# Optimization experiments

Measured on AMD Instinct MI355X. Metric: run time of the kernel, lower is better.

## Reference

```python
import jax, jax.numpy as jnp
import numpy as np

D_MODEL = 1024
N_HEADS = 16
D_K = D_MODEL // N_HEADS


def setup_inputs() -> dict:
    key = jax.random.key(0)
    ks = jax.random.split(key, 11)
    B, S = 2, 2048
    scale = 1.0 / np.sqrt(D_MODEL)
    return {
        "query": jax.random.normal(ks[0], (B, S, D_MODEL), jnp.float32),
        "key": jax.random.normal(ks[1], (B, S, D_MODEL), jnp.float32),
        "value": jax.random.normal(ks[2], (B, S, D_MODEL), jnp.float32),
        "w_q": jax.random.normal(ks[3], (D_MODEL, D_MODEL), jnp.float32) * scale,
        "b_q": jnp.zeros((D_MODEL,), jnp.float32),
        "w_k": jax.random.normal(ks[4], (D_MODEL, D_MODEL), jnp.float32) * scale,
        "b_k": jnp.zeros((D_MODEL,), jnp.float32),
        "w_v": jax.random.normal(ks[5], (D_MODEL, D_MODEL), jnp.float32) * scale,
        "b_v": jnp.zeros((D_MODEL,), jnp.float32),
        "w_o": jax.random.normal(ks[6], (D_MODEL, D_MODEL), jnp.float32) * scale,
        "b_o": jnp.zeros((D_MODEL,), jnp.float32),
    }


def reference(query, key, value, w_q, b_q, w_k, b_k, w_v, b_v, w_o, b_o):
    B, S, _ = query.shape
    # Linear projections (torch Linear: x @ W.T + b), split heads -> (B, H, S, Dk)
    def proj(x, w, b):
        y = jnp.einsum('bsd,ed->bse', x, w) + b
        return y.reshape(B, -1, N_HEADS, D_K).transpose(0, 2, 1, 3)
    q = proj(query, w_q, b_q)
    k = proj(key, w_k, b_k)
    v = proj(value, w_v, b_v)
    # Scaled dot-product attention (full O(S^2) scores, faithful to source)
    scores = jnp.einsum('bhqd,bhkd->bhqk', q, k) / np.sqrt(D_K)
    attn = jax.nn.softmax(scores, axis=-1)
    out = jnp.einsum('bhqk,bhkd->bhqd', attn, v)  # (B, H, S, Dk)
    out = out.transpose(0, 2, 1, 3).reshape(B, S, D_MODEL)
    out = jnp.einsum('bsd,ed->bse', out, w_o) + b_o
    return out
```

## Files before the change

### kernel.cpp

```cpp
#include <hip/hip_runtime.h>
#include <hip/hip_bf16.h>

#define DM 1024
#define NH 16
#define DKH 64
#define BB 2
#define SS 2048
#define MM (BB*SS)
#define HKB 1024

typedef __bf16 v8bf __attribute__((ext_vector_type(8)));
typedef float  v4f  __attribute__((ext_vector_type(4)));
typedef float  v16f __attribute__((ext_vector_type(16)));

__device__ __forceinline__ unsigned short f2bf(float f) {
    union { float f; unsigned int u; } v; v.f = f;
    unsigned int u = v.u;
    unsigned int r = (u + 0x7fffu + ((u >> 16) & 1u)) >> 16;
    return (unsigned short)r;
}

__device__ __forceinline__ int cvtpk(float lo, float hi) {
    int r;
    asm("v_cvt_pk_bf16_f32 %0, %1, %2" : "=v"(r) : "v"(lo), "v"(hi));
    return r;
}

__device__ __forceinline__ void pl32swap(int& a, int& b) {
    asm("v_permlane32_swap_b32 %0, %1" : "+v"(a), "+v"(b));
}

__device__ __forceinline__ void gl16(const unsigned short* g, unsigned short* l) {
    auto gp = reinterpret_cast<const __attribute__((address_space(1))) unsigned int*>(
        reinterpret_cast<uintptr_t>(g));
    auto lp = reinterpret_cast<__attribute__((address_space(3))) unsigned int*>(
        reinterpret_cast<uintptr_t>(l));
    __builtin_amdgcn_global_load_lds(gp, lp, 16, 0, 0);
}

__global__ __launch_bounds__(256) void cvt_to_bf16(
    const float* __restrict__ xq, const float* __restrict__ xk, const float* __restrict__ xv,
    const float* __restrict__ wq, const float* __restrict__ wk, const float* __restrict__ wv,
    const float* __restrict__ wo, unsigned short* __restrict__ dst)
{
    const int y = blockIdx.y;
    const float* src;
    size_t n, off;
    if (y < 3) {
        src = (y == 0) ? xq : (y == 1) ? xk : xv;
        n = (size_t)MM * DM;
        off = (size_t)y * MM * DM;
    } else {
        src = (y == 3) ? wq : (y == 4) ? wk : (y == 5) ? wv : wo;
        n = (size_t)DM * DM;
        off = (size_t)3 * MM * DM + (size_t)(y - 3) * DM * DM;
    }
    unsigned short* d = dst + off;
    const size_t stride = (size_t)gridDim.x * blockDim.x;
    for (size_t i = (size_t)blockIdx.x * blockDim.x + threadIdx.x; i * 8 < n; i += stride) {
        float4 a = ((const float4*)src)[2 * i];
        float4 b = ((const float4*)src)[2 * i + 1];
        uint4 o;
        o.x = (unsigned)cvtpk(a.x, a.y);
        o.y = (unsigned)cvtpk(a.z, a.w);
        o.z = (unsigned)cvtpk(b.x, b.y);
        o.w = (unsigned)cvtpk(b.z, b.w);
        ((uint4*)d)[i] = o;
    }
}

__global__ __launch_bounds__(256) void proj_qkv_b(
    const unsigned short* __restrict__ xb, const unsigned short* __restrict__ wb,
    const float* __restrict__ bq, const float* __restrict__ bk, const float* __restrict__ bv,
    unsigned short* __restrict__ q_ws, unsigned short* __restrict__ k_ws,
    unsigned short* __restrict__ vt_ws)
{
    const int z = blockIdx.z;
    const unsigned short* X = xb + (size_t)z * MM * DM;
    const unsigned short* W = wb + (size_t)z * DM * DM;
    const float* bias = (z == 0) ? bq : (z == 1) ? bk : bv;

    __shared__ unsigned short lA[2][128 * 32];
    __shared__ unsigned short lB[2][128 * 32];

    const int t = threadIdx.x;
    const int lane = t & 63, w = t >> 6;
    const int wm = w >> 1, wn = w & 1;
    const int g = lane >> 4, lr = lane & 15;

    const int hid = blockIdx.y * 8 + blockIdx.x;
    const int xcd = hid & 7, slot = hid >> 3;
    const int mbase = (xcd * 4 + (slot & 3)) * 128;
    const int nbase = (slot >> 2) * 128;

    const int srow = lane >> 2;
    const int scol = (lane & 3) * 8;

    v4f acc[4][4];
#pragma unroll
    for (int i = 0; i < 4; ++i)
#pragma unroll
        for (int j = 0; j < 4; ++j)
            acc[i][j] = (v4f){0.f, 0.f, 0.f, 0.f};

    auto stage = [&](int bi, int kb) {
        gl16(X + (size_t)(mbase + w * 16 + srow) * DM + kb + scol,      &lA[bi][w * 512]);
        gl16(X + (size_t)(mbase + 64 + w * 16 + srow) * DM + kb + scol, &lA[bi][(w + 4) * 512]);
        gl16(W + (size_t)(nbase + w * 16 + srow) * DM + kb + scol,      &lB[bi][w * 512]);
        gl16(W + (size_t)(nbase + 64 + w * 16 + srow) * DM + kb + scol, &lB[bi][(w + 4) * 512]);
    };

    stage(0, 0);
    __syncthreads();
    int buf = 0;
    for (int ki = 0; ki < 32; ++ki) {
        if (ki + 1 < 32) stage(buf ^ 1, (ki + 1) * 32);

        v8bf af[4], bf4[4];
#pragma unroll
        for (int mt = 0; mt < 4; ++mt)
            af[mt] = *(const v8bf*)(&lA[buf][(wm * 64 + mt * 16 + lr) * 32 + g * 8]);
#pragma unroll
        for (int nt = 0; nt < 4; ++nt)
            bf4[nt] = *(const v8bf*)(&lB[buf][(wn * 64 + nt * 16 + lr) * 32 + g * 8]);
#pragma unroll
        for (int mt = 0; mt < 4; ++mt)
#pragma unroll
            for (int nt = 0; nt < 4; ++nt)
                acc[mt][nt] = __builtin_amdgcn_mfma_f32_16x16x32_bf16(af[mt], bf4[nt], acc[mt][nt], 0, 0, 0);

        __syncthreads();
        buf ^= 1;
    }

    const float scale = (z == 0) ? 0.18033688011112042f : 1.0f;
#pragma unroll
    for (int nt = 0; nt < 4; ++nt) {
        int e = nbase + wn * 64 + nt * 16 + lr;
        float bval = bias[e];
        int h = e >> 6, dk = e & 63;
#pragma unroll
        for (int mt = 0; mt < 4; ++mt) {
#pragma unroll
            for (int r = 0; r < 4; ++r) {
                int m = mbase + wm * 64 + mt * 16 + g * 4 + r;
                float val = (acc[mt][nt][r] + bval) * scale;
                unsigned short o = f2bf(val);
                int b = m >> 11, s = m & 2047;
                if (z == 2) {
                    vt_ws[((size_t)(b * NH + h) * DKH + dk) * SS + s] = o;
                } else {
                    unsigned short* dst = (z == 0) ? q_ws : k_ws;
                    dst[((size_t)(b * NH + h) * SS + s) * DKH + dk] = o;
                }
            }
        }
    }
}

#define KB 64
#define LDP 72
#define TILE 4608

__global__ __launch_bounds__(512, 4) void attn_kernel(
    const unsigned short* __restrict__ q_ws, const unsigned short* __restrict__ k_ws,
    const unsigned short* __restrict__ vt_ws, unsigned short* __restrict__ o_ws)
{
    __shared__ __align__(16) unsigned short lsBuf[2 * 4 * TILE];

    const int t = threadIdx.x, l = t & 63, w = t >> 6;
    const int h = l >> 5, ql = l & 31;
    const int qg = w >> 1, hf = w & 1;

    const int hid = blockIdx.x;
    const int slot = hid >> 3;
    const int bh = (hid & 7) * 4 + (slot & 3);
    const int qp = slot >> 2;
    const int q0 = qp * 128 + qg * 32;

    const unsigned short* Kb = k_ws + (size_t)bh * SS * DKH;
    const unsigned short* Vb = vt_ws + (size_t)bh * DKH * SS;

    v8bf qf[4];
#pragma unroll
    for (int c = 0; c < 4; ++c)
        qf[c] = *(const v8bf*)(q_ws + ((size_t)bh * SS + q0 + ql) * DKH + c * 16 + h * 8);

    v16f oT[2];
#pragma unroll
    for (int d = 0; d < 2; ++d)
#pragma unroll
        for (int r = 0; r < 16; ++r) oT[d][r] = 0.f;
    float l_lane = 0.f;
    const v16f z16 = {};

    const int r0s = t >> 3, c0s = (t & 7) * 8;
    uint4 k0r, k1r, v0r, v1r;

    k0r = *(const uint4*)(Kb + (size_t)(r0s) * DKH + c0s);
    v0r = *(const uint4*)(Vb + (size_t)r0s * SS + c0s);
    k1r = *(const uint4*)(Kb + (size_t)(HKB + r0s) * DKH + c0s);
    v1r = *(const uint4*)(Vb + (size_t)r0s * SS + HKB + c0s);
    {
        unsigned short* B0 = lsBuf;
        *(uint4*)&B0[0 * TILE + r0s * LDP + c0s] = k0r;
        *(uint4*)&B0[1 * TILE + r0s * LDP + c0s] = v0r;
        *(uint4*)&B0[2 * TILE + r0s * LDP + c0s] = k1r;
        *(uint4*)&B0[3 * TILE + r0s * LDP + c0s] = v1r;
    }
    k0r = *(const uint4*)(Kb + (size_t)(KB + r0s) * DKH + c0s);
    v0r = *(const uint4*)(Vb + (size_t)r0s * SS + KB + c0s);
    k1r = *(const uint4*)(Kb + (size_t)(HKB + KB + r0s) * DKH + c0s);
    v1r = *(const uint4*)(Vb + (size_t)r0s * SS + HKB + KB + c0s);
    __syncthreads();

    const int NT = 16;
    int p = 0;
    for (int tt = 0; tt < NT; ++tt) {
        unsigned short* Kp = lsBuf + p * (4 * TILE) + hf * (2 * TILE);
        unsigned short* Vp = Kp + TILE;
        if (tt + 1 < NT) {
            unsigned short* Bn = lsBuf + (p ^ 1) * (4 * TILE);
            *(uint4*)&Bn[0 * TILE + r0s * LDP + c0s] = k0r;
            *(uint4*)&Bn[1 * TILE + r0s * LDP + c0s] = v0r;
            *(uint4*)&Bn[2 * TILE + r0s * LDP + c0s] = k1r;
            *(uint4*)&Bn[3 * TILE + r0s * LDP + c0s] = v1r;
        }
        if (tt + 2 < NT) {
            int kt2 = (tt + 2) * KB;
            k0r = *(const uint4*)(Kb + (size_t)(kt2 + r0s) * DKH + c0s);
            v0r = *(const uint4*)(Vb + (size_t)r0s * SS + kt2 + c0s);
            k1r = *(const uint4*)(Kb + (size_t)(HKB + kt2 + r0s) * DKH + c0s);
            v1r = *(const uint4*)(Vb + (size_t)r0s * SS + HKB + kt2 + c0s);
        }

        v16f sT[2];
        __builtin_amdgcn_s_setprio(1);
#pragma unroll
        for (int kb = 0; kb < 2; ++kb) {
            v8bf kf = *(const v8bf*)&Kp[(kb * 32 + ql) * LDP + h * 8];
            sT[kb] = __builtin_amdgcn_mfma_f32_32x32x16_bf16(kf, qf[0], z16, 0, 0, 0);
        }
#pragma unroll
        for (int c = 1; c < 4; ++c)
#pragma unroll
            for (int kb = 0; kb < 2; ++kb) {
                v8bf kf = *(const v8bf*)&Kp[(kb * 32 + ql) * LDP + c * 16 + h * 8];
                sT[kb] = __builtin_amdgcn_mfma_f32_32x32x16_bf16(kf, qf[c], sT[kb], 0, 0, 0);
            }
        __builtin_amdgcn_s_setprio(0);

        float rs0 = 0.f, rs1 = 0.f, rs2 = 0.f, rs3 = 0.f;
#pragma unroll
        for (int kb = 0; kb < 2; ++kb)
#pragma unroll
            for (int r = 0; r < 16; r += 4) {
                float e0 = __builtin_amdgcn_exp2f(sT[kb][r + 0]);
                float e1 = __builtin_amdgcn_exp2f(sT[kb][r + 1]);
                float e2 = __builtin_amdgcn_exp2f(sT[kb][r + 2]);
                float e3 = __builtin_amdgcn_exp2f(sT[kb][r + 3]);
                sT[kb][r + 0] = e0; sT[kb][r + 1] = e1;
                sT[kb][r + 2] = e2; sT[kb][r + 3] = e3;
                rs0 += e0; rs1 += e1; rs2 += e2; rs3 += e3;
            }
        l_lane += (rs0 + rs1) + (rs2 + rs3);

        v8bf pfrag[4];
#pragma unroll
        for (int c = 0; c < 4; ++c) {
            const int cc = c & 1, kb = c >> 1;
            int A0 = cvtpk(sT[kb][8 * cc + 0], sT[kb][8 * cc + 1]);
            int A1 = cvtpk(sT[kb][8 * cc + 2], sT[kb][8 * cc + 3]);
            int B0 = cvtpk(sT[kb][8 * cc + 4], sT[kb][8 * cc + 5]);
            int B1 = cvtpk(sT[kb][8 * cc + 6], sT[kb][8 * cc + 7]);
            pl32swap(A0, B0);
            pl32swap(A1, B1);
            union { int i[4]; v8bf v; } u;
            u.i[0] = A0; u.i[1] = A1; u.i[2] = B0; u.i[3] = B1;
            pfrag[c] = u.v;
        }

        __builtin_amdgcn_s_setprio(1);
#pragma unroll
        for (int db = 0; db < 2; ++db)
#pragma unroll
            for (int c = 0; c < 4; ++c) {
                v8bf vf = *(const v8bf*)&Vp[(db * 32 + ql) * LDP + c * 16 + h * 8];
                oT[db] = __builtin_amdgcn_mfma_f32_32x32x16_bf16(vf, pfrag[c], oT[db], 0, 0, 0);
            }
        __builtin_amdgcn_s_setprio(0);

        __syncthreads();
        p ^= 1;
    }

    float lsum = l_lane + __shfl_xor(l_lane, 32);
    float* lsf = (float*)lsBuf;
    const int row = qg * 32 + ql;
#pragma unroll
    for (int db = 0; db < 2; ++db)
#pragma unroll
        for (int r = 0; r < 16; ++r) {
            int d = db * 32 + (r & 3) + 8 * (r >> 2) + 4 * h;
            lsf[(hf * 128 + row) * 65 + d] = oT[db][r];
        }
    if (h == 0) lsf[(hf * 128 + row) * 65 + 64] = lsum;
    __syncthreads();

    const int orow = t >> 2;
    const int ck = t & 3;
    const float* e0 = lsf + orow * 65;
    const float* e1 = lsf + (128 + orow) * 65;
    const float linv = 1.0f / (e0[64] + e1[64]);
    const int b = bh >> 4, hh = bh & 15;
    const int d0 = ck * 16;
    unsigned short* op = o_ws + ((size_t)b * SS + qp * 128 + orow) * DM + hh * DKH + d0;
    uint4 o0, o1;
    o0.x = (unsigned)cvtpk((e0[d0+0]+e1[d0+0])*linv,  (e0[d0+1]+e1[d0+1])*linv);
    o0.y = (unsigned)cvtpk((e0[d0+2]+e1[d0+2])*linv,  (e0[d0+3]+e1[d0+3])*linv);
    o0.z = (unsigned)cvtpk((e0[d0+4]+e1[d0+4])*linv,  (e0[d0+5]+e1[d0+5])*linv);
    o0.w = (unsigned)cvtpk((e0[d0+6]+e1[d0+6])*linv,  (e0[d0+7]+e1[d0+7])*linv);
    o1.x = (unsigned)cvtpk((e0[d0+8]+e1[d0+8])*linv,  (e0[d0+9]+e1[d0+9])*linv);
    o1.y = (unsigned)cvtpk((e0[d0+10]+e1[d0+10])*linv,(e0[d0+11]+e1[d0+11])*linv);
    o1.z = (unsigned)cvtpk((e0[d0+12]+e1[d0+12])*linv,(e0[d0+13]+e1[d0+13])*linv);
    o1.w = (unsigned)cvtpk((e0[d0+14]+e1[d0+14])*linv,(e0[d0+15]+e1[d0+15])*linv);
    *(uint4*)op = o0;
    *(uint4*)(op + 8) = o1;
}

__global__ __launch_bounds__(256) void proj_o_b(
    const unsigned short* __restrict__ A, const unsigned short* __restrict__ W,
    const float* __restrict__ bo, float* __restrict__ out)
{
    __shared__ unsigned short lA[2][128 * 32];
    __shared__ unsigned short lB[2][128 * 32];

    const int t = threadIdx.x;
    const int lane = t & 63, w = t >> 6;
    const int wm = w >> 1, wn = w & 1;
    const int g = lane >> 4, lr = lane & 15;

    const int hid = blockIdx.y * 8 + blockIdx.x;
    const int xcd = hid & 7, slot = hid >> 3;
    const int mbase = (xcd * 4 + (slot & 3)) * 128;
    const int nbase = (slot >> 2) * 128;

    const int srow = lane >> 2;
    const int scol = (lane & 3) * 8;

    v4f acc[4][4];
#pragma unroll
    for (int i = 0; i < 4; ++i)
#pragma unroll
        for (int j = 0; j < 4; ++j)
            acc[i][j] = (v4f){0.f, 0.f, 0.f, 0.f};

    auto stage = [&](int bi, int kb) {
        gl16(A + (size_t)(mbase + w * 16 + srow) * DM + kb + scol,      &lA[bi][w * 512]);
        gl16(A + (size_t)(mbase + 64 + w * 16 + srow) * DM + kb + scol, &lA[bi][(w + 4) * 512]);
        gl16(W + (size_t)(nbase + w * 16 + srow) * DM + kb + scol,      &lB[bi][w * 512]);
        gl16(W + (size_t)(nbase + 64 + w * 16 + srow) * DM + kb + scol, &lB[bi][(w + 4) * 512]);
    };

    stage(0, 0);
    __syncthreads();
    int buf = 0;
    for (int ki = 0; ki < 32; ++ki) {
        if (ki + 1 < 32) stage(buf ^ 1, (ki + 1) * 32);

        v8bf af[4], bf4[4];
#pragma unroll
        for (int mt = 0; mt < 4; ++mt)
            af[mt] = *(const v8bf*)(&lA[buf][(wm * 64 + mt * 16 + lr) * 32 + g * 8]);
#pragma unroll
        for (int nt = 0; nt < 4; ++nt)
            bf4[nt] = *(const v8bf*)(&lB[buf][(wn * 64 + nt * 16 + lr) * 32 + g * 8]);
#pragma unroll
        for (int mt = 0; mt < 4; ++mt)
#pragma unroll
            for (int nt = 0; nt < 4; ++nt)
                acc[mt][nt] = __builtin_amdgcn_mfma_f32_16x16x32_bf16(af[mt], bf4[nt], acc[mt][nt], 0, 0, 0);

        __syncthreads();
        buf ^= 1;
    }

#pragma unroll
    for (int nt = 0; nt < 4; ++nt) {
        int e = nbase + wn * 64 + nt * 16 + lr;
        float bval = bo[e];
#pragma unroll
        for (int mt = 0; mt < 4; ++mt) {
#pragma unroll
            for (int r = 0; r < 4; ++r) {
                int m = mbase + wm * 64 + mt * 16 + g * 4 + r;
                out[(size_t)m * DM + e] = acc[mt][nt][r] + bval;
            }
        }
    }
}

extern "C" void kernel_launch(void* const* d_in, const int* in_sizes, int n_in,
                              void* d_out, int out_size, void* d_ws, size_t ws_size,
                              hipStream_t stream) {
    const float* q  = (const float*)d_in[0];
    const float* k  = (const float*)d_in[1];
    const float* v  = (const float*)d_in[2];
    const float* wq = (const float*)d_in[3];
    const float* bq = (const float*)d_in[4];
    const float* wk = (const float*)d_in[5];
    const float* bk = (const float*)d_in[6];
    const float* wv = (const float*)d_in[7];
    const float* bv = (const float*)d_in[8];
    const float* wo = (const float*)d_in[9];
    const float* bo = (const float*)d_in[10];
    float* out = (float*)d_out;

    unsigned short* ws    = (unsigned short*)d_ws;
    unsigned short* q_ws  = ws;
    unsigned short* k_ws  = q_ws + (size_t)MM * DM;
    unsigned short* vt_ws = k_ws + (size_t)MM * DM;
    unsigned short* xb    = vt_ws + (size_t)MM * DM;
    unsigned short* wb    = xb + (size_t)3 * MM * DM;
    unsigned short* o_ws  = xb;

    cvt_to_bf16<<<dim3(256, 7), 256, 0, stream>>>(q, k, v, wq, wk, wv, wo, xb);
    proj_qkv_b<<<dim3(8, 32, 3), 256, 0, stream>>>(xb, wb, bq, bk, bv, q_ws, k_ws, vt_ws);
    attn_kernel<<<dim3(512), 512, 0, stream>>>(q_ws, k_ws, vt_ws, o_ws);
    proj_o_b<<<dim3(8, 32), 256, 0, stream>>>(o_ws, wb + (size_t)3 * DM * DM, bo, out);
}
```

Baseline: 128.8 us.

## Triple-buffer projection GEMM loads and halve output-projection N tile

Both projection GEMMs move from a double-buffered loop with a full __syncthreads per step to a three-stage LDS ring. Two tiles stay in flight, and explicit s_waitcnt vmcnt counts plus s_barrier wait only for the tile being consumed. The output projection also drops its N tile from 128 to 64 and launches twice as many blocks, so 256 blocks become 512 for better CU occupancy. The costs are more shared memory per block and lower per-block data reuse in the output projection. The correctness of the hand-counted vmcnt values depends on gl16 issuing exactly one vector memory op per call.

```diff
diff --git a/kernel.cpp b/kernel.cpp
--- a/kernel.cpp
+++ b/kernel.cpp
@@ -80,8 +80,8 @@
     const unsigned short* W = wb + (size_t)z * DM * DM;
     const float* bias = (z == 0) ? bq : (z == 1) ? bk : bv;
 
-    __shared__ unsigned short lA[2][128 * 32];
-    __shared__ unsigned short lB[2][128 * 32];
+    __shared__ unsigned short lA[3][128 * 32];
+    __shared__ unsigned short lB[3][128 * 32];
 
     const int t = threadIdx.x;
     const int lane = t & 63, w = t >> 6;
@@ -109,29 +109,50 @@
         gl16(W + (size_t)(nbase + w * 16 + srow) * DM + kb + scol,      &lB[bi][w * 512]);
         gl16(W + (size_t)(nbase + 64 + w * 16 + srow) * DM + kb + scol, &lB[bi][(w + 4) * 512]);
     };
-
-    stage(0, 0);
-    __syncthreads();
-    int buf = 0;
-    for (int ki = 0; ki < 32; ++ki) {
-        if (ki + 1 < 32) stage(buf ^ 1, (ki + 1) * 32);
-
+    auto compute = [&](int bi) {
         v8bf af[4], bf4[4];
 #pragma unroll
         for (int mt = 0; mt < 4; ++mt)
-            af[mt] = *(const v8bf*)(&lA[buf][(wm * 64 + mt * 16 + lr) * 32 + g * 8]);
+            af[mt] = *(const v8bf*)(&lA[bi][(wm * 64 + mt * 16 + lr) * 32 + g * 8]);
 #pragma unroll
         for (int nt = 0; nt < 4; ++nt)
-            bf4[nt] = *(const v8bf*)(&lB[buf][(wn * 64 + nt * 16 + lr) * 32 + g * 8]);
+            bf4[nt] = *(const v8bf*)(&lB[bi][(wn * 64 + nt * 16 + lr) * 32 + g * 8]);
 #pragma unroll
         for (int mt = 0; mt < 4; ++mt)
 #pragma unroll
             for (int nt = 0; nt < 4; ++nt)
                 acc[mt][nt] = __builtin_amdgcn_mfma_f32_16x16x32_bf16(af[mt], bf4[nt], acc[mt][nt], 0, 0, 0);
-
-        __syncthreads();
-        buf ^= 1;
-    }
+    };
+
+    stage(0, 0);
+    stage(1, 32);
+    int bcur = 0;
+#pragma unroll 1
+    for (int ki = 0; ki < 30; ++ki) {
+        int bnext = bcur + 2; if (bnext >= 3) bnext -= 3;
+        stage(bnext, (ki + 2) * 32);
+        asm volatile("s_waitcnt vmcnt(8)" ::: "memory");
+        __builtin_amdgcn_sched_barrier(0);
+        __builtin_amdgcn_s_barrier();
+        __builtin_amdgcn_sched_barrier(0);
+        compute(bcur);
+        __builtin_amdgcn_sched_barrier(0);
+        __builtin_amdgcn_s_barrier();
+        bcur = (bcur == 2) ? 0 : bcur + 1;
+    }
+    asm volatile("s_waitcnt vmcnt(4)" ::: "memory");
+    __builtin_amdgcn_sched_barrier(0);
+    __builtin_amdgcn_s_barrier();
+    __builtin_amdgcn_sched_barrier(0);
+    compute(bcur);
+    __builtin_amdgcn_sched_barrier(0);
+    __builtin_amdgcn_s_barrier();
+    bcur = (bcur == 2) ? 0 : bcur + 1;
+    asm volatile("s_waitcnt vmcnt(0)" ::: "memory");
+    __builtin_amdgcn_sched_barrier(0);
+    __builtin_amdgcn_s_barrier();
+    __builtin_amdgcn_sched_barrier(0);
+    compute(bcur);
 
     const float scale = (z == 0) ? 0.18033688011112042f : 1.0f;
 #pragma unroll
@@ -332,62 +353,82 @@
     const unsigned short* __restrict__ A, const unsigned short* __restrict__ W,
     const float* __restrict__ bo, float* __restrict__ out)
 {
-    __shared__ unsigned short lA[2][128 * 32];
-    __shared__ unsigned short lB[2][128 * 32];
+    __shared__ unsigned short lA[3][128 * 32];
+    __shared__ unsigned short lB[3][64 * 32];
 
     const int t = threadIdx.x;
     const int lane = t & 63, w = t >> 6;
     const int wm = w >> 1, wn = w & 1;
     const int g = lane >> 4, lr = lane & 15;
 
-    const int hid = blockIdx.y * 8 + blockIdx.x;
+    const int hid = blockIdx.y * 16 + blockIdx.x;
     const int xcd = hid & 7, slot = hid >> 3;
     const int mbase = (xcd * 4 + (slot & 3)) * 128;
-    const int nbase = (slot >> 2) * 128;
+    const int nbase = (slot >> 2) * 64;
 
     const int srow = lane >> 2;
     const int scol = (lane & 3) * 8;
 
-    v4f acc[4][4];
+    v4f acc[4][2];
 #pragma unroll
     for (int i = 0; i < 4; ++i)
 #pragma unroll
-        for (int j = 0; j < 4; ++j)
+        for (int j = 0; j < 2; ++j)
             acc[i][j] = (v4f){0.f, 0.f, 0.f, 0.f};
 
     auto stage = [&](int bi, int kb) {
         gl16(A + (size_t)(mbase + w * 16 + srow) * DM + kb + scol,      &lA[bi][w * 512]);
         gl16(A + (size_t)(mbase + 64 + w * 16 + srow) * DM + kb + scol, &lA[bi][(w + 4) * 512]);
         gl16(W + (size_t)(nbase + w * 16 + srow) * DM + kb + scol,      &lB[bi][w * 512]);
-        gl16(W + (size_t)(nbase + 64 + w * 16 + srow) * DM + kb + scol, &lB[bi][(w + 4) * 512]);
     };
+    auto compute = [&](int bi) {
+        v8bf af[4], bf4[2];
+#pragma unroll
+        for (int mt = 0; mt < 4; ++mt)
+            af[mt] = *(const v8bf*)(&lA[bi][(wm * 64 + mt * 16 + lr) * 32 + g * 8]);
+#pragma unroll
+        for (int nt = 0; nt < 2; ++nt)
+            bf4[nt] = *(const v8bf*)(&lB[bi][(wn * 32 + nt * 16 + lr) * 32 + g * 8]);
+#pragma unroll
+        for (int mt = 0; mt < 4; ++mt)
+#pragma unroll
+            for (int nt = 0; nt < 2; ++nt)
+                acc[mt][nt] = __builtin_amdgcn_mfma_f32_16x16x32_bf16(af[mt], bf4[nt], acc[mt][nt], 0, 0, 0);
+    };
 
     stage(0, 0);
-    __syncthreads();
-    int buf = 0;
-    for (int ki = 0; ki < 32; ++ki) {
-        if (ki + 1 < 32) stage(buf ^ 1, (ki + 1) * 32);
-
-        v8bf af[4], bf4[4];
-#pragma unroll
-        for (int mt = 0; mt < 4; ++mt)
-            af[mt] = *(const v8bf*)(&lA[buf][(wm * 64 + mt * 16 + lr) * 32 + g * 8]);
-#pragma unroll
-        for (int nt = 0; nt < 4; ++nt)
-            bf4[nt] = *(const v8bf*)(&lB[buf][(wn * 64 + nt * 16 + lr) * 32 + g * 8]);
-#pragma unroll
-        for (int mt = 0; mt < 4; ++mt)
-#pragma unroll
-            for (int nt = 0; nt < 4; ++nt)
-                acc[mt][nt] = __builtin_amdgcn_mfma_f32_16x16x32_bf16(af[mt], bf4[nt], acc[mt][nt], 0, 0, 0);
-
-        __syncthreads();
-        buf ^= 1;
-    }
-
-#pragma unroll
-    for (int nt = 0; nt < 4; ++nt) {
-        int e = nbase + wn * 64 + nt * 16 + lr;
+    stage(1, 32);
+    int bcur = 0;
+#pragma unroll 1
+    for (int ki = 0; ki < 30; ++ki) {
+        int bnext = bcur + 2; if (bnext >= 3) bnext -= 3;
+        stage(bnext, (ki + 2) * 32);
+        asm volatile("s_waitcnt vmcnt(6)" ::: "memory");
+        __builtin_amdgcn_sched_barrier(0);
+        __builtin_amdgcn_s_barrier();
+        __builtin_amdgcn_sched_barrier(0);
+        compute(bcur);
+        __builtin_amdgcn_sched_barrier(0);
+        __builtin_amdgcn_s_barrier();
+        bcur = (bcur == 2) ? 0 : bcur + 1;
+    }
+    asm volatile("s_waitcnt vmcnt(3)" ::: "memory");
+    __builtin_amdgcn_sched_barrier(0);
+    __builtin_amdgcn_s_barrier();
+    __builtin_amdgcn_sched_barrier(0);
+    compute(bcur);
+    __builtin_amdgcn_sched_barrier(0);
+    __builtin_amdgcn_s_barrier();
+    bcur = (bcur == 2) ? 0 : bcur + 1;
+    asm volatile("s_waitcnt vmcnt(0)" ::: "memory");
+    __builtin_amdgcn_sched_barrier(0);
+    __builtin_amdgcn_s_barrier();
+    __builtin_amdgcn_sched_barrier(0);
+    compute(bcur);
+
+#pragma unroll
+    for (int nt = 0; nt < 2; ++nt) {
+        int e = nbase + wn * 32 + nt * 16 + lr;
         float bval = bo[e];
 #pragma unroll
         for (int mt = 0; mt < 4; ++mt) {
@@ -427,5 +468,5 @@
     cvt_to_bf16<<<dim3(256, 7), 256, 0, stream>>>(q, k, v, wq, wk, wv, wo, xb);
     proj_qkv_b<<<dim3(8, 32, 3), 256, 0, stream>>>(xb, wb, bq, bk, bv, q_ws, k_ws, vt_ws);
     attn_kernel<<<dim3(512), 512, 0, stream>>>(q_ws, k_ws, vt_ws, o_ws);
-    proj_o_b<<<dim3(8, 32), 256, 0, stream>>>(o_ws, wb + (size_t)3 * DM * DM, bo, out);
-}
+    proj_o_b<<<dim3(16, 32), 256, 0, stream>>>(o_ws, wb + (size_t)3 * DM * DM, bo, out);
+}
```

After: 120.4 us. 1.07x faster.
